# Kernel tuning notes

Hardware: AMD Instinct MI355X
Metric: run time of the kernel (lower is better)

## Reference

```python
import jax, jax.numpy as jnp
import numpy as np


def _ln(x, g, b):
    m = x.mean(-1, keepdims=True)
    v = ((x - m) ** 2).mean(-1, keepdims=True)
    return (x - m) * jax.lax.rsqrt(v + 1e-5) * g + b


def _forward(x, fx_in, pre_w1, pre_b1, pre_w2, pre_b2, placeholder,
             ln1_g, ln1_b, px_w, px_b, pfx_w, pfx_b, slice_w, slice_b, temp,
             q_w, k_w, v_w, out_w, out_b, ln2_g, ln2_b,
             mlp_w1, mlp_b1, mlp_w2, mlp_b2,
             ln3_g, ln3_b, head_w1, head_b1, head_w2, head_b2):
    # All linear weights are stored as [in, out] (pre-transposed vs torch nn.Linear).
    B, N, _ = x.shape
    L, H = temp.shape
    dh = slice_w.shape[1]
    gelu = lambda t: jax.nn.gelu(t, approximate=False)
    # preprocess MLP (n_layers=0, res=False): Linear -> GELU -> Linear
    h = jnp.concatenate([x, fx_in], axis=-1)
    h = gelu(h @ pre_w1 + pre_b1) @ pre_w2 + pre_b2
    h = h + placeholder  # learned [D] offset
    scale = 1.0 / jnp.sqrt(jnp.asarray(dh, h.dtype))
    for i in range(L):  # loop over structurally distinct layers
        y = _ln(h, ln1_g[i], ln1_b[i])
        # project to per-head features: bhnd
        fx_mid = (y @ pfx_w[i] + pfx_b[i]).reshape(B, N, H, dh).transpose(0, 2, 1, 3)
        x_mid = (y @ px_w[i] + px_b[i]).reshape(B, N, H, dh).transpose(0, 2, 1, 3)
        # soft slice assignment over G slices
        logits = jnp.einsum('bhnd,dg->bhng', x_mid, slice_w[i]) + slice_b[i]
        sw = jax.nn.softmax(logits / temp[i][None, :, None, None], axis=-1)  # bhng
        norm = sw.sum(axis=2)  # bhg
        tok = jnp.einsum('bhnd,bhng->bhgd', fx_mid, sw) / (norm + 1e-5)[..., None]
        # attention over G=slice_num tokens
        q = tok @ q_w[i]
        k = tok @ k_w[i]
        v = tok @ v_w[i]
        attn = jax.nn.softmax(jnp.einsum('bhgd,bhmd->bhgm', q, k) * scale, axis=-1)
        out_slice = jnp.einsum('bhgm,bhmd->bhgd', attn, v)
        # deslice back to points
        out_x = jnp.einsum('bhgd,bhng->bhnd', out_slice, sw)
        out_x = out_x.transpose(0, 2, 1, 3).reshape(B, N, H * dh)
        h = h + (out_x @ out_w[i] + out_b[i])
        z = _ln(h, ln2_g[i], ln2_b[i])
        h = h + (gelu(z @ mlp_w1[i] + mlp_b1[i]) @ mlp_w2[i] + mlp_b2[i])
    z = _ln(h, ln3_g, ln3_b)
    return gelu(z @ head_w1 + head_b1) @ head_w2 + head_b2


def setup_inputs() -> dict:
    key = jax.random.key(0)
    B, N, D, H, dh, G, L = 2, 16384, 256, 8, 32, 64, 5
    SP, FUN, OUT = 2, 4, 4
    ID = H * dh  # inner_dim == n_hidden
    MR = D * 1   # mlp_ratio=1
    ks = iter(jax.random.split(key, 64))
    nrm = lambda shape, s=0.02: jax.random.normal(next(ks), shape, jnp.float32) * s
    return dict(
        x=jax.random.normal(next(ks), (B, N, SP), jnp.float32),
        fx_in=jax.random.normal(next(ks), (B, N, FUN), jnp.float32),
        pre_w1=nrm((SP + FUN, 2 * D)), pre_b1=jnp.zeros((2 * D,), jnp.float32),
        pre_w2=nrm((2 * D, D)), pre_b2=jnp.zeros((D,), jnp.float32),
        placeholder=nrm((D,)),
        ln1_g=jnp.ones((L, D), jnp.float32), ln1_b=jnp.zeros((L, D), jnp.float32),
        px_w=nrm((L, D, ID)), px_b=jnp.zeros((L, ID), jnp.float32),
        pfx_w=nrm((L, D, ID)), pfx_b=jnp.zeros((L, ID), jnp.float32),
        slice_w=nrm((L, dh, G), 0.1), slice_b=jnp.zeros((L, G), jnp.float32),
        temp=0.5 * jnp.ones((L, H), jnp.float32),
        q_w=nrm((L, dh, dh), 0.1), k_w=nrm((L, dh, dh), 0.1), v_w=nrm((L, dh, dh), 0.1),
        out_w=nrm((L, ID, D)), out_b=jnp.zeros((L, D), jnp.float32),
        ln2_g=jnp.ones((L, D), jnp.float32), ln2_b=jnp.zeros((L, D), jnp.float32),
        mlp_w1=nrm((L, D, MR)), mlp_b1=jnp.zeros((L, MR), jnp.float32),
        mlp_w2=nrm((L, MR, D)), mlp_b2=jnp.zeros((L, D), jnp.float32),
        ln3_g=jnp.ones((D,), jnp.float32), ln3_b=jnp.zeros((D,), jnp.float32),
        head_w1=nrm((D, D)), head_b1=jnp.zeros((D,), jnp.float32),
        head_w2=nrm((D, OUT)), head_b2=jnp.zeros((OUT,), jnp.float32),
    )


def reference(x, fx_in, pre_w1, pre_b1, pre_w2, pre_b2, placeholder,
              ln1_g, ln1_b, px_w, px_b, pfx_w, pfx_b, slice_w, slice_b, temp,
              q_w, k_w, v_w, out_w, out_b, ln2_g, ln2_b,
              mlp_w1, mlp_b1, mlp_w2, mlp_b2,
              ln3_g, ln3_b, head_w1, head_b1, head_w2, head_b2):
    return _forward(x, fx_in, pre_w1, pre_b1, pre_w2, pre_b2, placeholder,
                    ln1_g, ln1_b, px_w, px_b, pfx_w, pfx_b, slice_w, slice_b, temp,
                    q_w, k_w, v_w, out_w, out_b, ln2_g, ln2_b,
                    mlp_w1, mlp_b1, mlp_w2, mlp_b2,
                    ln3_g, ln3_b, head_w1, head_b1, head_w2, head_b2)
```

## Files before the change

kernel.cpp:

```cpp
#include <hip/hip_runtime.h>


#define MTOK 32768
#define NB   16384

typedef unsigned short u16;
using short8 = __attribute__((ext_vector_type(8))) short;
using f4     = __attribute__((ext_vector_type(4))) float;

__device__ __forceinline__ float bfu(u16 u) {
    return __uint_as_float(((unsigned)u) << 16);
}
__device__ __forceinline__ u16 f2bf(float f) {
    unsigned u = __float_as_uint(f);
    u += 0x7FFFu + ((u >> 16) & 1u);
    return (u16)(u >> 16);
}
__device__ __forceinline__ float ldf(const void* p, int i, int isbf) {
    return isbf ? bfu(((const u16*)p)[i]) : ((const float*)p)[i];
}
__device__ __forceinline__ float4 dec4(ushort4 u) {
    return make_float4(bfu(u.x), bfu(u.y), bfu(u.z), bfu(u.w));
}
__device__ __forceinline__ float gelu_f(float x) {
    return 0.5f * x * (1.0f + erff(x * 0.7071067811865475f));
}

#define F_H      ((size_t)0)
#define F_TOK    ((size_t)8388608)
#define F_NORM   ((size_t)8421376)
#define F_OS     ((size_t)8422400)
#define F_BIAS   ((size_t)8455168)
#define F_PARAMS ((size_t)8463360)
#define F_BF     ((size_t)8696196)
#define B_PB2C 0
#define B_PFXB 256
#define B_OUTB 1536
#define B_M1B  2816
#define B_M2B  4096
#define B_HB1  5376
#define B_SL   5632
#define B_END  8192
#define U_WT     ((size_t)0)
#define WT_PRE2  0
#define WT_HEAD1 131072
#define WT_PXSL  196608
#define WT_PFX   851968
#define WT_OUT   1179648
#define WT_MLP1  1507328
#define WT_MLP2  1835008
#define WT_END   2162688
#define U_Y   ((size_t)2162688)
#define U_XM  ((size_t)10551296)
#define U_FM  ((size_t)18939904)
#define U_SW  ((size_t)27328512)

#define P_X    0
#define P_FX   65536
#define P_W1   196608
#define P_B1   199680
#define P_LN1G 200192
#define P_LN1B 201472
#define P_LN2G 202752
#define P_LN2B 204032
#define P_LN3G 205312
#define P_LN3B 205568
#define P_SLW  205824
#define P_SLB  216064
#define P_TEMP 216384
#define P_QW   216448
#define P_KW   221568
#define P_VW   226688
#define P_HW2  231808
#define P_HB2  232832
#define P_END  232836

__global__ __launch_bounds__(256) void cvt_kernel(
    const void* x, const void* fx, const void* w1, const void* b1,
    const void* l1g, const void* l1b, const void* l2g, const void* l2b,
    const void* l3g, const void* l3b, const void* slw, const void* slb,
    const void* tmp, const void* qw, const void* kw, const void* vw,
    const void* hw2, const void* hb2, float* __restrict__ P)
{
    int isbf = (((const u16*)tmp)[0] != 0);
    int idx = blockIdx.x * 256 + threadIdx.x;
    const void* s; int o;
    if      (idx < 65536)  { s = x;   o = idx; }
    else if (idx < 196608) { s = fx;  o = idx - 65536; }
    else if (idx < 199680) { s = w1;  o = idx - 196608; }
    else if (idx < 200192) { s = b1;  o = idx - 199680; }
    else if (idx < 201472) { s = l1g; o = idx - 200192; }
    else if (idx < 202752) { s = l1b; o = idx - 201472; }
    else if (idx < 204032) { s = l2g; o = idx - 202752; }
    else if (idx < 205312) { s = l2b; o = idx - 204032; }
    else if (idx < 205568) { s = l3g; o = idx - 205312; }
    else if (idx < 205824) { s = l3b; o = idx - 205568; }
    else if (idx < 216064) { s = slw; o = idx - 205824; }
    else if (idx < 216384) { s = slb; o = idx - 216064; }
    else if (idx < 216424) { s = tmp; o = idx - 216384; }
    else if (idx < 216448) { return; }
    else if (idx < 221568) { s = qw;  o = idx - 216448; }
    else if (idx < 226688) { s = kw;  o = idx - 221568; }
    else if (idx < 231808) { s = vw;  o = idx - 226688; }
    else if (idx < 232832) { s = hw2; o = idx - 231808; }
    else if (idx < 232836) { s = hb2; o = idx - 232832; }
    else return;
    P[idx] = ldf(s, o, isbf);
}

__global__ __launch_bounds__(256) void prep_kernel(
    const void* pre_w2, const void* head_w1, const void* px_w, const void* pfx_w,
    const void* out_w, const void* mlp_w1, const void* mlp_w2, const void* pre_b2,
    const void* placeholder, const void* px_b, const void* pfx_b, const void* out_b,
    const void* mlp_b1, const void* mlp_b2, const void* head_b1,
    const void* slw, const void* slb, const void* tmp,
    u16* __restrict__ WT, float* __restrict__ BIAS)
{
    int isbf = (((const u16*)tmp)[0] != 0);
    int idx = blockIdx.x * 256 + threadIdx.x;
    if (idx < 131072) {
        int n = idx >> 9, k = idx & 511;
        WT[idx] = f2bf(ldf(pre_w2, k * 256 + n, isbf));
    } else if (idx < WT_PXSL) {
        int f = idx - 131072;
        int n = f >> 8, k = f & 255;
        WT[idx] = f2bf(ldf(head_w1, k * 256 + n, isbf));
    } else if (idx < WT_PFX) {
        int f = idx - WT_PXSL;
        int i = f / 131072, r = f % 131072;
        int n = r >> 8, k = r & 255;
        int h = n >> 6, g = n & 63;
        float a = 0.f;
#pragma unroll
        for (int d = 0; d < 32; ++d)
            a = fmaf(ldf(px_w, i * 65536 + k * 256 + h * 32 + d, isbf),
                     ldf(slw, i * 2048 + d * 64 + g, isbf), a);
        WT[idx] = f2bf(a);
    } else if (idx < WT_END) {
        int f = idx - WT_PFX;
        int mat = f >> 16;
        int r = f & 65535;
        const void* s; int off = (mat % 5) * 65536;
        if      (mat < 5)  s = pfx_w;
        else if (mat < 10) s = out_w;
        else if (mat < 15) s = mlp_w1;
        else               s = mlp_w2;
        int n = r >> 8, k = r & 255;
        WT[idx] = f2bf(ldf(s, off + k * 256 + n, isbf));
    } else if (idx < WT_END + 256) {
        int c = idx - WT_END;
        BIAS[B_PB2C + c] = ldf(pre_b2, c, isbf) + ldf(placeholder, c, isbf);
    } else if (idx < WT_END + B_SL) {
        int o = idx - (WT_END + 256);
        float v;
        if      (o < 1280) v = ldf(pfx_b,  o,        isbf);
        else if (o < 2560) v = ldf(out_b,  o - 1280, isbf);
        else if (o < 3840) v = ldf(mlp_b1, o - 2560, isbf);
        else if (o < 5120) v = ldf(mlp_b2, o - 3840, isbf);
        else               v = ldf(head_b1, o - 5120, isbf);
        BIAS[B_PFXB + o] = v;
    } else if (idx < WT_END + B_END) {
        int o = idx - (WT_END + B_SL);
        int i = o >> 9, n = o & 511;
        int h = n >> 6, g = n & 63;
        float a = ldf(slb, i * 64 + g, isbf);
#pragma unroll
        for (int d = 0; d < 32; ++d)
            a = fmaf(ldf(px_b, i * 256 + h * 32 + d, isbf),
                     ldf(slw, i * 2048 + d * 64 + g, isbf), a);
        BIAS[B_SL + o] = a;
    }
}

__global__ __launch_bounds__(256) void pre1_kernel(
    const float* __restrict__ P, u16* __restrict__ HID)
{
    int idx = blockIdx.x * 256 + threadIdx.x;
    int m = idx >> 9, j = idx & 511;
    const float* xx = P + P_X;
    const float* ff = P + P_FX;
    const float* w1 = P + P_W1;
    float a = P[P_B1 + j];
    a = fmaf(xx[m * 2 + 0], w1[0 * 512 + j], a);
    a = fmaf(xx[m * 2 + 1], w1[1 * 512 + j], a);
    a = fmaf(ff[m * 4 + 0], w1[2 * 512 + j], a);
    a = fmaf(ff[m * 4 + 1], w1[3 * 512 + j], a);
    a = fmaf(ff[m * 4 + 2], w1[4 * 512 + j], a);
    a = fmaf(ff[m * 4 + 3], w1[5 * 512 + j], a);
    HID[idx] = f2bf(gelu_f(a));
}

template <int KK, int OMODE>
__global__ __launch_bounds__(256, 2) void gemm_mfma(
    const u16* __restrict__ A, const u16* __restrict__ Wt,
    const float* __restrict__ bias, float* __restrict__ C, u16* __restrict__ Cb)
{
    __shared__ u16 As[128 * 72];
    __shared__ u16 Bs[128 * 72];
    const int t = threadIdx.x;
    const int wave = t >> 6, lane = t & 63;
    const int quad = lane >> 4, l15 = lane & 15;
    const int m0 = blockIdx.x * 128;
    const int n0 = blockIdx.y * 128;
    const int wm = (wave & 1) * 64, wn = (wave >> 1) * 64;
    f4 acc[4][4];
#pragma unroll
    for (int i = 0; i < 4; ++i)
#pragma unroll
        for (int j = 0; j < 4; ++j)
            acc[i][j] = (f4){0.f, 0.f, 0.f, 0.f};

    for (int kc = 0; kc < KK; kc += 64) {
        if (kc) __syncthreads();
#pragma unroll
        for (int i = 0; i < 4; ++i) {
            int c = t + 256 * i;
            int row = c >> 3, col = (c & 7) * 8;
            *(ulonglong2*)(As + row * 72 + col) =
                *(const ulonglong2*)(A + (size_t)(m0 + row) * KK + kc + col);
            *(ulonglong2*)(Bs + row * 72 + col) =
                *(const ulonglong2*)(Wt + (size_t)(n0 + row) * KK + kc + col);
        }
        __syncthreads();
#pragma unroll
        for (int k32 = 0; k32 < 64; k32 += 32) {
            short8 a[4], b[4];
#pragma unroll
            for (int i = 0; i < 4; ++i)
                a[i] = *(const short8*)(As + (wm + i * 16 + l15) * 72 + k32 + quad * 8);
#pragma unroll
            for (int j = 0; j < 4; ++j)
                b[j] = *(const short8*)(Bs + (wn + j * 16 + l15) * 72 + k32 + quad * 8);
#pragma unroll
            for (int i = 0; i < 4; ++i)
#pragma unroll
                for (int j = 0; j < 4; ++j)
                    acc[i][j] = __builtin_amdgcn_mfma_f32_16x16x32_bf16(
                        a[i], b[j], acc[i][j], 0, 0, 0);
        }
    }
#pragma unroll
    for (int j = 0; j < 4; ++j) {
        int cj = n0 + wn + j * 16 + l15;
        float bj = bias[cj];
#pragma unroll
        for (int i = 0; i < 4; ++i) {
            int rbase = m0 + wm + i * 16 + quad * 4;
#pragma unroll
            for (int r = 0; r < 4; ++r) {
                float v = acc[i][j][r] + bj;
                size_t off = (size_t)(rbase + r) * 256 + cj;
                if (OMODE == 3) v = gelu_f(v);
                if (OMODE == 1) v += C[off];
                if (OMODE >= 2) Cb[off] = f2bf(v);
                else            C[off] = v;
            }
        }
    }
}

__global__ __launch_bounds__(256, 2) void gemm_slice(
    const u16* __restrict__ A, const u16* __restrict__ Wt,
    const float* __restrict__ bsl, const float* __restrict__ tempv,
    u16* __restrict__ SW)
{
    __shared__ u16 As[128 * 72];
    __shared__ u16 Bs[128 * 72];
    const int t = threadIdx.x;
    const int wave = t >> 6, lane = t & 63;
    const int quad = lane >> 4, l15 = lane & 15;
    const int m0 = blockIdx.x * 128;
    const int n0 = blockIdx.y * 128;
    const int wm = (wave & 1) * 64, wn = (wave >> 1) * 64;
    f4 acc[4][4];
#pragma unroll
    for (int i = 0; i < 4; ++i)
#pragma unroll
        for (int j = 0; j < 4; ++j)
            acc[i][j] = (f4){0.f, 0.f, 0.f, 0.f};

    for (int kc = 0; kc < 256; kc += 64) {
        if (kc) __syncthreads();
#pragma unroll
        for (int i = 0; i < 4; ++i) {
            int c = t + 256 * i;
            int row = c >> 3, col = (c & 7) * 8;
            *(ulonglong2*)(As + row * 72 + col) =
                *(const ulonglong2*)(A + (size_t)(m0 + row) * 256 + kc + col);
            *(ulonglong2*)(Bs + row * 72 + col) =
                *(const ulonglong2*)(Wt + (size_t)(n0 + row) * 256 + kc + col);
        }
        __syncthreads();
#pragma unroll
        for (int k32 = 0; k32 < 64; k32 += 32) {
            short8 a[4], b[4];
#pragma unroll
            for (int i = 0; i < 4; ++i)
                a[i] = *(const short8*)(As + (wm + i * 16 + l15) * 72 + k32 + quad * 8);
#pragma unroll
            for (int j = 0; j < 4; ++j)
                b[j] = *(const short8*)(Bs + (wn + j * 16 + l15) * 72 + k32 + quad * 8);
#pragma unroll
            for (int i = 0; i < 4; ++i)
#pragma unroll
                for (int j = 0; j < 4; ++j)
                    acc[i][j] = __builtin_amdgcn_mfma_f32_16x16x32_bf16(
                        a[i], b[j], acc[i][j], 0, 0, 0);
        }
    }
    const int h = (n0 + wn) >> 6;
    const float itemp = 1.0f / tempv[h];
    float bj[4];
#pragma unroll
    for (int j = 0; j < 4; ++j) bj[j] = bsl[n0 + wn + j * 16 + l15];
#pragma unroll
    for (int i = 0; i < 4; ++i) {
#pragma unroll
        for (int r = 0; r < 4; ++r) {
            float v[4];
            float mx = -3.0e38f;
#pragma unroll
            for (int j = 0; j < 4; ++j) {
                v[j] = (acc[i][j][r] + bj[j]) * itemp;
                mx = fmaxf(mx, v[j]);
            }
#pragma unroll
            for (int o = 1; o < 16; o <<= 1) mx = fmaxf(mx, __shfl_xor(mx, o));
            float s = 0.f;
#pragma unroll
            for (int j = 0; j < 4; ++j) { v[j] = expf(v[j] - mx); s += v[j]; }
#pragma unroll
            for (int o = 1; o < 16; o <<= 1) s += __shfl_xor(s, o);
            float inv = 1.0f / s;
            int m = m0 + wm + i * 16 + quad * 4 + r;
            int b = m >> 14, n = m & 16383;
            size_t base = (((size_t)(b * 8 + h)) * NB + n) * 64;
#pragma unroll
            for (int j = 0; j < 4; ++j)
                SW[base + j * 16 + l15] = f2bf(v[j] * inv);
        }
    }
}

__global__ __launch_bounds__(256) void ln_kernel(
    const float* __restrict__ X, const float* __restrict__ g,
    const float* __restrict__ b, u16* __restrict__ Y)
{
    int lane = threadIdx.x & 63;
    size_t m = (size_t)blockIdx.x * 4 + (threadIdx.x >> 6);
    const float4 x4 = *(const float4*)(X + m * 256 + lane * 4);
    float s = x4.x + x4.y + x4.z + x4.w;
    float q = x4.x * x4.x + x4.y * x4.y + x4.z * x4.z + x4.w * x4.w;
#pragma unroll
    for (int o = 32; o; o >>= 1) { s += __shfl_xor(s, o); q += __shfl_xor(q, o); }
    float mean = s * (1.0f / 256.0f);
    float var = q * (1.0f / 256.0f) - mean * mean;
    float inv = 1.0f / sqrtf(var + 1e-5f);
    const float4 g4 = *(const float4*)(g + lane * 4);
    const float4 b4 = *(const float4*)(b + lane * 4);
    ushort4 y;
    y.x = f2bf((x4.x - mean) * inv * g4.x + b4.x);
    y.y = f2bf((x4.y - mean) * inv * g4.y + b4.y);
    y.z = f2bf((x4.z - mean) * inv * g4.z + b4.z);
    y.w = f2bf((x4.w - mean) * inv * g4.w + b4.w);
    *(ushort4*)(Y + m * 256 + lane * 4) = y;
}

__global__ __launch_bounds__(256) void tok_kernel(
    const u16* __restrict__ FM, const u16* __restrict__ SW,
    float* __restrict__ TOK, float* __restrict__ NORM)
{
    int bh = blockIdx.x >> 6, chunk = blockIdx.x & 63;
    int b = bh >> 3, hd = bh & 7;
    int t = threadIdx.x, wave = t >> 6, lane = t & 63;
    int g0 = (lane >> 3) * 8, d0 = (lane & 7) * 4;
    float4 acc[8];
#pragma unroll
    for (int gi = 0; gi < 8; ++gi) acc[gi] = make_float4(0.f, 0.f, 0.f, 0.f);
    float4 n0a = make_float4(0.f, 0.f, 0.f, 0.f);
    float4 n1a = make_float4(0.f, 0.f, 0.f, 0.f);
    int nbase = chunk * 256 + wave * 64;
    const u16* fmB = FM + ((size_t)b * NB + nbase) * 256 + hd * 32 + d0;
    const u16* swB = SW + ((size_t)bh * NB + nbase) * 64 + g0;
    for (int j = 0; j < 64; ++j) {
        float4 f4v = dec4(*(const ushort4*)(fmB + (size_t)j * 256));
        float4 s0 = dec4(*(const ushort4*)(swB + (size_t)j * 64));
        float4 s1 = dec4(*(const ushort4*)(swB + (size_t)j * 64 + 4));
#define TOKACC(gi, sv)                                            \
        acc[gi].x = fmaf(f4v.x, sv, acc[gi].x);                   \
        acc[gi].y = fmaf(f4v.y, sv, acc[gi].y);                   \
        acc[gi].z = fmaf(f4v.z, sv, acc[gi].z);                   \
        acc[gi].w = fmaf(f4v.w, sv, acc[gi].w);
        TOKACC(0, s0.x) TOKACC(1, s0.y) TOKACC(2, s0.z) TOKACC(3, s0.w)
        TOKACC(4, s1.x) TOKACC(5, s1.y) TOKACC(6, s1.z) TOKACC(7, s1.w)
#undef TOKACC
        n0a.x += s0.x; n0a.y += s0.y; n0a.z += s0.z; n0a.w += s0.w;
        n1a.x += s1.x; n1a.y += s1.y; n1a.z += s1.z; n1a.w += s1.w;
    }
    __shared__ float red[4][2048];
    __shared__ float nred[4][64];
#pragma unroll
    for (int gi = 0; gi < 8; ++gi)
        *(float4*)&red[wave][(g0 + gi) * 32 + d0] = acc[gi];
    if ((lane & 7) == 0) {
        nred[wave][g0 + 0] = n0a.x; nred[wave][g0 + 1] = n0a.y;
        nred[wave][g0 + 2] = n0a.z; nred[wave][g0 + 3] = n0a.w;
        nred[wave][g0 + 4] = n1a.x; nred[wave][g0 + 5] = n1a.y;
        nred[wave][g0 + 6] = n1a.z; nred[wave][g0 + 7] = n1a.w;
    }
    __syncthreads();
    size_t tokBase = (size_t)bh * 2048;
#pragma unroll
    for (int k = 0; k < 8; ++k) {
        int c = t + 256 * k;
        atomicAdd(&TOK[tokBase + c], red[0][c] + red[1][c] + red[2][c] + red[3][c]);
    }
    if (t < 64)
        atomicAdd(&NORM[bh * 64 + t], nred[0][t] + nred[1][t] + nred[2][t] + nred[3][t]);
}

__global__ __launch_bounds__(256) void attn_kernel(
    const float* __restrict__ TOK, const float* __restrict__ NORM,
    const float* __restrict__ qw, const float* __restrict__ kw,
    const float* __restrict__ vw, float* __restrict__ OS)
{
    __shared__ float tokd[2048], qs[2048], ks[2048], vs[2048];
    int bh = blockIdx.x;
    int t = threadIdx.x;
#pragma unroll
    for (int i = 0; i < 2; ++i) {
        int f4v = t + 256 * i;
        float4 v = *(const float4*)(TOK + (size_t)bh * 2048 + f4v * 4);
        float inv = 1.0f / (NORM[bh * 64 + (f4v >> 3)] + 1e-5f);
        v.x *= inv; v.y *= inv; v.z *= inv; v.w *= inv;
        *(float4*)&tokd[f4v * 4] = v;
    }
    __syncthreads();
#pragma unroll
    for (int i = 0; i < 8; ++i) {
        int f = t + 256 * i;
        int g = f >> 5, d = f & 31;
        const float* tr = tokd + g * 32;
        float aq = 0.f, ak = 0.f, av = 0.f;
#pragma unroll
        for (int e = 0; e < 32; ++e) {
            float tv = tr[e];
            aq = fmaf(tv, qw[e * 32 + d], aq);
            ak = fmaf(tv, kw[e * 32 + d], ak);
            av = fmaf(tv, vw[e * 32 + d], av);
        }
        qs[f] = aq; ks[f] = ak; vs[f] = av;
    }
    __syncthreads();
    int g = t >> 2, sub = t & 3;
    float4 qv[8];
#pragma unroll
    for (int e4 = 0; e4 < 8; ++e4) qv[e4] = *(const float4*)(qs + g * 32 + e4 * 4);
    float p[16];
    float mx = -3.0e38f;
#pragma unroll
    for (int mm = 0; mm < 16; ++mm) {
        int mI = sub * 16 + mm;
        const float4* kr = (const float4*)(ks + mI * 32);
        float s = 0.f;
#pragma unroll
        for (int e4 = 0; e4 < 8; ++e4) {
            float4 kv = kr[e4];
            s = fmaf(qv[e4].x, kv.x, s); s = fmaf(qv[e4].y, kv.y, s);
// ... 105 lines not shown
        if (isbf) {
            ushort4 r; r.x = f2bf(o0); r.y = f2bf(o1); r.z = f2bf(o2); r.w = f2bf(o3);
            *(ushort4*)((u16*)OUT + m * 4) = r;
        } else {
            *(float4*)((float*)OUT + m * 4) = make_float4(o0, o1, o2, o3);
        }
    }
}

extern "C" void kernel_launch(void* const* d_in, const int* in_sizes, int n_in,
                              void* d_out, int out_size, void* d_ws, size_t ws_size,
                              hipStream_t stream)
{
    const void* x = d_in[0];      const void* fx = d_in[1];
    const void* pre_w1 = d_in[2]; const void* pre_b1 = d_in[3];
    const void* pre_w2 = d_in[4]; const void* pre_b2 = d_in[5];
    const void* placeholder = d_in[6];
    const void* ln1_g = d_in[7];  const void* ln1_b = d_in[8];
    const void* px_w = d_in[9];   const void* px_b = d_in[10];
    const void* pfx_w = d_in[11]; const void* pfx_b = d_in[12];
    const void* slice_w = d_in[13]; const void* slice_b = d_in[14];
    const void* temp = d_in[15];
    const void* q_w = d_in[16];   const void* k_w = d_in[17]; const void* v_w = d_in[18];
    const void* out_w = d_in[19]; const void* out_b = d_in[20];
    const void* ln2_g = d_in[21]; const void* ln2_b = d_in[22];
    const void* mlp_w1 = d_in[23]; const void* mlp_b1 = d_in[24];
    const void* mlp_w2 = d_in[25]; const void* mlp_b2 = d_in[26];
    const void* ln3_g = d_in[27]; const void* ln3_b = d_in[28];
    const void* head_w1 = d_in[29]; const void* head_b1 = d_in[30];
    const void* head_w2 = d_in[31]; const void* head_b2 = d_in[32];

    float* ws = (float*)d_ws;
    float* H     = ws + F_H;
    float* TOKp  = ws + F_TOK;
    float* NORMp = ws + F_NORM;
    float* OSp   = ws + F_OS;
    float* BIAS  = ws + F_BIAS;
    float* P     = ws + F_PARAMS;
    u16*   U     = (u16*)(ws + F_BF);
    u16*   WT    = U + U_WT;
    u16*   Yb    = U + U_Y;
    u16*   XMb   = U + U_XM;
    u16*   FMb   = U + U_FM;
    u16*   SWb   = U + U_SW;
    u16*   HIDb  = U + U_XM;

    cvt_kernel<<<910, 256, 0, stream>>>(x, fx, pre_w1, pre_b1, ln1_g, ln1_b,
        ln2_g, ln2_b, ln3_g, ln3_b, slice_w, slice_b, temp, q_w, k_w, v_w,
        head_w2, head_b2, P);
    prep_kernel<<<8480, 256, 0, stream>>>(pre_w2, head_w1, px_w, pfx_w, out_w,
        mlp_w1, mlp_w2, pre_b2, placeholder, px_b, pfx_b, out_b, mlp_b1, mlp_b2,
        head_b1, slice_w, slice_b, temp, WT, BIAS);
    pre1_kernel<<<65536, 256, 0, stream>>>(P, HIDb);

    dim3 gg(256, 2);
    dim3 gs(256, 4);
    gemm_mfma<512, 0><<<gg, 256, 0, stream>>>(HIDb, WT + WT_PRE2, BIAS + B_PB2C, H, nullptr);

    for (int i = 0; i < 5; ++i) {
        ln_kernel<<<8192, 256, 0, stream>>>(H, P + P_LN1G + i * 256, P + P_LN1B + i * 256, Yb);
        gemm_slice<<<gs, 256, 0, stream>>>(Yb, WT + WT_PXSL + i * 131072, BIAS + B_SL + i * 512, P + P_TEMP + i * 8, SWb);
        gemm_mfma<256, 2><<<gg, 256, 0, stream>>>(Yb, WT + WT_PFX + i * 65536, BIAS + B_PFXB + i * 256, nullptr, FMb);
        hipMemsetAsync(TOKp, 0, (size_t)33792 * 4, stream);
        tok_kernel<<<1024, 256, 0, stream>>>(FMb, SWb, TOKp, NORMp);
        attn_kernel<<<16, 256, 0, stream>>>(TOKp, NORMp, P + P_QW + i * 1024, P + P_KW + i * 1024, P + P_VW + i * 1024, OSp);
        deslice_kernel<<<2048, 256, 0, stream>>>(OSp, SWb, Yb);
        gemm_mfma<256, 1><<<gg, 256, 0, stream>>>(Yb, WT + WT_OUT + i * 65536, BIAS + B_OUTB + i * 256, H, nullptr);
        ln_kernel<<<8192, 256, 0, stream>>>(H, P + P_LN2G + i * 256, P + P_LN2B + i * 256, Yb);
        gemm_mfma<256, 3><<<gg, 256, 0, stream>>>(Yb,  WT + WT_MLP1 + i * 65536, BIAS + B_M1B + i * 256, nullptr, XMb);
        gemm_mfma<256, 1><<<gg, 256, 0, stream>>>(XMb, WT + WT_MLP2 + i * 65536, BIAS + B_M2B + i * 256, H, nullptr);
    }

    ln_kernel<<<8192, 256, 0, stream>>>(H, P + P_LN3G, P + P_LN3B, Yb);
    gemm_mfma<256, 3><<<gg, 256, 0, stream>>>(Yb, WT + WT_HEAD1, BIAS + B_HB1, nullptr, XMb);
    head2_kernel<<<8192, 256, 0, stream>>>(XMb, P + P_HW2, P + P_HB2, temp, d_out);
}
```

Baseline: 1.265 ms.

## Fuse layernorm into GEMM epilogues, merge slice/fx projections, drop token atomics

Residual GEMMs now compute full 256-wide rows per block, so the following LayerNorm runs in the epilogue and the standalone ln_kernel launches go away. The slice-logit and fx projections are merged into one GEMM with a concatenated weight. Token reduction writes per-chunk partials that attn_kernel sums, replacing the memset and atomics. Also adds an XOR-swizzled LDS layout, vectorized pre1, and a tiled weight-prep kernel. The risks are lower occupancy from the wider GEMM tiles and the extra partial-sum reads in attn.

New measurement: 1.851 ms. 1.46x slower.

```diff
diff --git a/kernel.cpp b/kernel.cpp
--- a/kernel.cpp
+++ b/kernel.cpp
@@ -27,25 +27,23 @@
 }
 
 #define F_H      ((size_t)0)
-#define F_TOK    ((size_t)8388608)
-#define F_NORM   ((size_t)8421376)
-#define F_OS     ((size_t)8422400)
-#define F_BIAS   ((size_t)8455168)
-#define F_PARAMS ((size_t)8463360)
-#define F_BF     ((size_t)8696196)
+#define F_OS     ((size_t)8388608)
+#define F_TOKP   ((size_t)8421376)
+#define F_NORMP  ((size_t)8945664)
+#define F_BIAS   ((size_t)8962048)
+#define F_PARAMS ((size_t)8970240)
+#define F_BF     ((size_t)9203076)
 #define B_PB2C 0
-#define B_PFXB 256
-#define B_OUTB 1536
-#define B_M1B  2816
-#define B_M2B  4096
-#define B_HB1  5376
-#define B_SL   5632
+#define B_OUTB 256
+#define B_M1B  1536
+#define B_M2B  2816
+#define B_HB1  4096
+#define B_SP   4352
 #define B_END  8192
 #define U_WT     ((size_t)0)
 #define WT_PRE2  0
 #define WT_HEAD1 131072
-#define WT_PXSL  196608
-#define WT_PFX   851968
+#define WT_SPFX  196608
 #define WT_OUT   1179648
 #define WT_MLP1  1507328
 #define WT_MLP2  1835008
@@ -108,95 +106,238 @@
     P[idx] = ldf(s, o, isbf);
 }
 
-__global__ __launch_bounds__(256) void prep_kernel(
-    const void* pre_w2, const void* head_w1, const void* px_w, const void* pfx_w,
-    const void* out_w, const void* mlp_w1, const void* mlp_w2, const void* pre_b2,
-    const void* placeholder, const void* px_b, const void* pfx_b, const void* out_b,
-    const void* mlp_b1, const void* mlp_b2, const void* head_b1,
-    const void* slw, const void* slb, const void* tmp,
+__global__ __launch_bounds__(256) void prep_main(
+    const void* pre_w2, const void* head_w1, const void* pfx_w,
+    const void* out_w, const void* mlp_w1, const void* mlp_w2,
+    const void* pre_b2, const void* placeholder, const void* pfx_b,
+    const void* out_b, const void* mlp_b1, const void* mlp_b2,
+    const void* head_b1, const void* tmp,
     u16* __restrict__ WT, float* __restrict__ BIAS)
 {
     int isbf = (((const u16*)tmp)[0] != 0);
     int idx = blockIdx.x * 256 + threadIdx.x;
     if (idx < 131072) {
         int n = idx >> 9, k = idx & 511;
-        WT[idx] = f2bf(ldf(pre_w2, k * 256 + n, isbf));
-    } else if (idx < WT_PXSL) {
+        WT[WT_PRE2 + idx] = f2bf(ldf(pre_w2, k * 256 + n, isbf));
+    } else if (idx < 196608) {
         int f = idx - 131072;
         int n = f >> 8, k = f & 255;
-        WT[idx] = f2bf(ldf(head_w1, k * 256 + n, isbf));
-    } else if (idx < WT_PFX) {
-        int f = idx - WT_PXSL;
-        int i = f / 131072, r = f % 131072;
+        WT[WT_HEAD1 + f] = f2bf(ldf(head_w1, k * 256 + n, isbf));
+    } else if (idx < 524288) {
+        int f = idx - 196608;
+        int i = f >> 16, r = f & 65535;
         int n = r >> 8, k = r & 255;
-        int h = n >> 6, g = n & 63;
-        float a = 0.f;
-#pragma unroll
-        for (int d = 0; d < 32; ++d)
-            a = fmaf(ldf(px_w, i * 65536 + k * 256 + h * 32 + d, isbf),
-                     ldf(slw, i * 2048 + d * 64 + g, isbf), a);
-        WT[idx] = f2bf(a);
-    } else if (idx < WT_END) {
-        int f = idx - WT_PFX;
-        int mat = f >> 16;
-        int r = f & 65535;
+        WT[WT_SPFX + (size_t)i * 196608 + (512 + n) * 256 + k] =
+            f2bf(ldf(pfx_w, i * 65536 + k * 256 + n, isbf));
+    } else if (idx < 1507328) {
+        int f = idx - 524288;
+        int mat = f >> 16, r = f & 65535;
         const void* s; int off = (mat % 5) * 65536;
-        if      (mat < 5)  s = pfx_w;
-        else if (mat < 10) s = out_w;
-        else if (mat < 15) s = mlp_w1;
+        if      (mat < 5)  s = out_w;
+        else if (mat < 10) s = mlp_w1;
         else               s = mlp_w2;
         int n = r >> 8, k = r & 255;
-        WT[idx] = f2bf(ldf(s, off + k * 256 + n, isbf));
-    } else if (idx < WT_END + 256) {
-        int c = idx - WT_END;
+        WT[WT_OUT + f] = f2bf(ldf(s, off + k * 256 + n, isbf));
+    } else if (idx < 1507584) {
+        int c = idx - 1507328;
         BIAS[B_PB2C + c] = ldf(pre_b2, c, isbf) + ldf(placeholder, c, isbf);
-    } else if (idx < WT_END + B_SL) {
-        int o = idx - (WT_END + 256);
-        float v;
-        if      (o < 1280) v = ldf(pfx_b,  o,        isbf);
-        else if (o < 2560) v = ldf(out_b,  o - 1280, isbf);
-        else if (o < 3840) v = ldf(mlp_b1, o - 2560, isbf);
-        else if (o < 5120) v = ldf(mlp_b2, o - 3840, isbf);
-        else               v = ldf(head_b1, o - 5120, isbf);
-        BIAS[B_PFXB + o] = v;
-    } else if (idx < WT_END + B_END) {
-        int o = idx - (WT_END + B_SL);
-        int i = o >> 9, n = o & 511;
-        int h = n >> 6, g = n & 63;
+    } else if (idx < 1508864) {
+        int o = idx - 1507584; BIAS[B_OUTB + o] = ldf(out_b, o, isbf);
+    } else if (idx < 1510144) {
+        int o = idx - 1508864; BIAS[B_M1B + o] = ldf(mlp_b1, o, isbf);
+    } else if (idx < 1511424) {
+        int o = idx - 1510144; BIAS[B_M2B + o] = ldf(mlp_b2, o, isbf);
+    } else if (idx < 1511680) {
+        int o = idx - 1511424; BIAS[B_HB1 + o] = ldf(head_b1, o, isbf);
+    } else if (idx < 1512960) {
+        int o = idx - 1511680;
+        int i = o >> 8, c = o & 255;
+        BIAS[B_SP + i * 768 + 512 + c] = ldf(pfx_b, o, isbf);
+    }
+}
+
+__global__ __launch_bounds__(256) void prep_pxsl(
+    const void* px_w, const void* px_b, const void* slw, const void* slb,
+    const void* tmp, u16* __restrict__ WT, float* __restrict__ BIAS)
+{
+    int isbf = (((const u16*)tmp)[0] != 0);
+    __shared__ float pxs[64 * 33];
+    __shared__ float sls[2048];
+    int blk = blockIdx.x;
+    int i = blk >> 5, h = (blk >> 2) & 7, kb = blk & 3;
+    int t = threadIdx.x;
+#pragma unroll
+    for (int p = 0; p < 8; ++p) {
+        int flat = t + 256 * p;
+        sls[flat] = ldf(slw, i * 2048 + flat, isbf);
+        int k = flat >> 5, d = flat & 31;
+        pxs[k * 33 + d] = ldf(px_w, i * 65536 + (kb * 64 + k) * 256 + h * 32 + d, isbf);
+    }
+    __syncthreads();
+    int k = t & 63, gb = t >> 6;
+    float acc[16];
+#pragma unroll
+    for (int gi = 0; gi < 16; ++gi) acc[gi] = 0.f;
+#pragma unroll
+    for (int d = 0; d < 32; ++d) {
+        float pv = pxs[k * 33 + d];
+        const float* sp = sls + d * 64 + gb * 16;
+#pragma unroll
+        for (int gi = 0; gi < 16; ++gi) acc[gi] = fmaf(pv, sp[gi], acc[gi]);
+    }
+    u16* WTp = WT + WT_SPFX + (size_t)i * 196608;
+#pragma unroll
+    for (int gi = 0; gi < 16; ++gi) {
+        int n = h * 64 + gb * 16 + gi;
+        WTp[n * 256 + kb * 64 + k] = f2bf(acc[gi]);
+    }
+    if (kb == 0 && t < 64) {
+        int g = t;
         float a = ldf(slb, i * 64 + g, isbf);
 #pragma unroll
         for (int d = 0; d < 32; ++d)
-            a = fmaf(ldf(px_b, i * 256 + h * 32 + d, isbf),
-                     ldf(slw, i * 2048 + d * 64 + g, isbf), a);
-        BIAS[B_SL + o] = a;
+            a = fmaf(ldf(px_b, i * 256 + h * 32 + d, isbf), sls[d * 64 + g], a);
+        BIAS[B_SP + i * 768 + h * 64 + g] = a;
     }
 }
 
 __global__ __launch_bounds__(256) void pre1_kernel(
     const float* __restrict__ P, u16* __restrict__ HID)
 {
-    int idx = blockIdx.x * 256 + threadIdx.x;
-    int m = idx >> 9, j = idx & 511;
-    const float* xx = P + P_X;
-    const float* ff = P + P_FX;
+    int base = (blockIdx.x * 256 + threadIdx.x) * 8;
+    int m = base >> 9, j0 = base & 511;
     const float* w1 = P + P_W1;
-    float a = P[P_B1 + j];
-    a = fmaf(xx[m * 2 + 0], w1[0 * 512 + j], a);
-    a = fmaf(xx[m * 2 + 1], w1[1 * 512 + j], a);
-    a = fmaf(ff[m * 4 + 0], w1[2 * 512 + j], a);
-    a = fmaf(ff[m * 4 + 1], w1[3 * 512 + j], a);
-    a = fmaf(ff[m * 4 + 2], w1[4 * 512 + j], a);
-    a = fmaf(ff[m * 4 + 3], w1[5 * 512 + j], a);
-    HID[idx] = f2bf(gelu_f(a));
-}
-
-template <int KK, int OMODE>
-__global__ __launch_bounds__(256, 2) void gemm_mfma(
+    float xa = P[P_X + m * 2], xb = P[P_X + m * 2 + 1];
+    float fa = P[P_FX + m * 4], fb = P[P_FX + m * 4 + 1];
+    float fc = P[P_FX + m * 4 + 2], fd = P[P_FX + m * 4 + 3];
+    u16 outv[8];
+#pragma unroll
+    for (int jj = 0; jj < 8; ++jj) {
+        int j = j0 + jj;
+        float a = P[P_B1 + j];
+        a = fmaf(xa, w1[j], a);
+        a = fmaf(xb, w1[512 + j], a);
+        a = fmaf(fa, w1[1024 + j], a);
+        a = fmaf(fb, w1[1536 + j], a);
+        a = fmaf(fc, w1[2048 + j], a);
+        a = fmaf(fd, w1[2560 + j], a);
+        outv[jj] = f2bf(gelu_f(a));
+    }
+    *(ushort4*)(HID + base)     = make_ushort4(outv[0], outv[1], outv[2], outv[3]);
+    *(ushort4*)(HID + base + 4) = make_ushort4(outv[4], outv[5], outv[6], outv[7]);
+}
+
+template <int KK, bool RES>
+__global__ __launch_bounds__(256, 3) void gemm_ln(
     const u16* __restrict__ A, const u16* __restrict__ Wt,
-    const float* __restrict__ bias, float* __restrict__ C, u16* __restrict__ Cb)
-{
-    __shared__ u16 As[128 * 72];
-    __shared__ u16 Bs[128 * 72];
+    const float* __restrict__ bias, const float* __restrict__ lng,
+    const float* __restrict__ lnb, float* __restrict__ H, u16* __restrict__ Y)
+{
+    __shared__ u16 As[64 * 64];
+    __shared__ u16 Bs[256 * 64];
+    __shared__ float rs[2][64], rq[2][64];
+    const int t = threadIdx.x;
+    const int wave = t >> 6, lane = t & 63;
+    const int quad = lane >> 4, l15 = lane & 15;
+    const int m0 = blockIdx.x * 64;
+    const int wm = (wave & 1) * 32, wn = (wave >> 1) * 128;
+    f4 acc[2][8];
+#pragma unroll
+    for (int i = 0; i < 2; ++i)
+#pragma unroll
+        for (int j = 0; j < 8; ++j) acc[i][j] = (f4){0.f, 0.f, 0.f, 0.f};
+
+    for (int kc = 0; kc < KK; kc += 64) {
+        if (kc) __syncthreads();
+#pragma unroll
+        for (int p = 0; p < 2; ++p) {
+            int c = t + 256 * p;
+            int row = c >> 3, c8 = c & 7;
+            *(ulonglong2*)(As + row * 64 + ((c8 ^ (row & 7)) << 3)) =
+                *(const ulonglong2*)(A + (size_t)(m0 + row) * KK + kc + c8 * 8);
+        }
+#pragma unroll
+        for (int p = 0; p < 8; ++p) {
+            int c = t + 256 * p;
+            int row = c >> 3, c8 = c & 7;
+            *(ulonglong2*)(Bs + row * 64 + ((c8 ^ (row & 7)) << 3)) =
+                *(const ulonglong2*)(Wt + (size_t)row * KK + kc + c8 * 8);
+        }
+        __syncthreads();
+#pragma unroll
+        for (int kk = 0; kk < 2; ++kk) {
+            short8 a[2], b[8];
+#pragma unroll
+            for (int i = 0; i < 2; ++i) {
+                int R = wm + i * 16 + l15;
+                a[i] = *(const short8*)(As + R * 64 + (((quad + kk * 4) ^ (R & 7)) << 3));
+            }
+#pragma unroll
+            for (int j = 0; j < 8; ++j) {
+                int R = wn + j * 16 + l15;
+                b[j] = *(const short8*)(Bs + R * 64 + (((quad + kk * 4) ^ (R & 7)) << 3));
+            }
+#pragma unroll
+            for (int i = 0; i < 2; ++i)
+#pragma unroll
+                for (int j = 0; j < 8; ++j)
+                    acc[i][j] = __builtin_amdgcn_mfma_f32_16x16x32_bf16(
+                        a[i], b[j], acc[i][j], 0, 0, 0);
+        }
+    }
+    float bj[8];
+    int colj[8];
+#pragma unroll
+    for (int j = 0; j < 8; ++j) { colj[j] = wn + j * 16 + l15; bj[j] = bias[colj[j]]; }
+    const int half = wn >> 7;
+#pragma unroll
+    for (int i = 0; i < 2; ++i) {
+#pragma unroll
+        for (int r = 0; r < 4; ++r) {
+            int row = wm + i * 16 + quad * 4 + r;
+            size_t gbase = (size_t)(m0 + row) * 256;
+            float s = 0.f, q = 0.f;
+#pragma unroll
+            for (int j = 0; j < 8; ++j) {
+                float v = acc[i][j][r] + bj[j];
+                if (RES) v += H[gbase + colj[j]];
+                H[gbase + colj[j]] = v;
+                acc[i][j][r] = v;
+                s += v; q += v * v;
+            }
+#pragma unroll
+            for (int o = 1; o < 16; o <<= 1) { s += __shfl_xor(s, o); q += __shfl_xor(q, o); }
+            if (l15 == 0) { rs[half][row] = s; rq[half][row] = q; }
+        }
+    }
+    __syncthreads();
+    float gj[8], betj[8];
+#pragma unroll
+    for (int j = 0; j < 8; ++j) { gj[j] = lng[colj[j]]; betj[j] = lnb[colj[j]]; }
+#pragma unroll
+    for (int i = 0; i < 2; ++i) {
+#pragma unroll
+        for (int r = 0; r < 4; ++r) {
+            int row = wm + i * 16 + quad * 4 + r;
+            size_t gbase = (size_t)(m0 + row) * 256;
+            float mean = (rs[0][row] + rs[1][row]) * (1.0f / 256.0f);
+            float var = (rq[0][row] + rq[1][row]) * (1.0f / 256.0f) - mean * mean;
+            float rstd = rsqrtf(var + 1e-5f);
+#pragma unroll
+            for (int j = 0; j < 8; ++j) {
+                float y = (acc[i][j][r] - mean) * rstd * gj[j] + betj[j];
+                Y[gbase + colj[j]] = f2bf(y);
+            }
+        }
+    }
+}
+
+__global__ __launch_bounds__(256, 4) void gemm_gelu(
+    const u16* __restrict__ A, const u16* __restrict__ Wt,
+    const float* __restrict__ bias, u16* __restrict__ Cb)
+{
+    __shared__ u16 As[128 * 64];
+    __shared__ u16 Bs[128 * 64];
     const int t = threadIdx.x;
     const int wave = t >> 6, lane = t & 63;
     const int quad = lane >> 4, l15 = lane & 15;
@@ -207,30 +348,34 @@
 #pragma unroll
     for (int i = 0; i < 4; ++i)
 #pragma unroll
-        for (int j = 0; j < 4; ++j)
-            acc[i][j] = (f4){0.f, 0.f, 0.f, 0.f};
-
-    for (int kc = 0; kc < KK; kc += 64) {
+        for (int j = 0; j < 4; ++j) acc[i][j] = (f4){0.f, 0.f, 0.f, 0.f};
+
+    for (int kc = 0; kc < 256; kc += 64) {
         if (kc) __syncthreads();
 #pragma unroll
-        for (int i = 0; i < 4; ++i) {
-            int c = t + 256 * i;
-            int row = c >> 3, col = (c & 7) * 8;
-            *(ulonglong2*)(As + row * 72 + col) =
-                *(const ulonglong2*)(A + (size_t)(m0 + row) * KK + kc + col);
-            *(ulonglong2*)(Bs + row * 72 + col) =
-                *(const ulonglong2*)(Wt + (size_t)(n0 + row) * KK + kc + col);
+        for (int p = 0; p < 4; ++p) {
+            int c = t + 256 * p;
+            int row = c >> 3, c8 = c & 7;
+            int off = row * 64 + ((c8 ^ (row & 7)) << 3);
+            *(ulonglong2*)(As + off) =
+                *(const ulonglong2*)(A + (size_t)(m0 + row) * 256 + kc + c8 * 8);
+            *(ulonglong2*)(Bs + off) =
+                *(const ulonglong2*)(Wt + (size_t)(n0 + row) * 256 + kc + c8 * 8);
         }
         __syncthreads();
 #pragma unroll
-        for (int k32 = 0; k32 < 64; k32 += 32) {
+        for (int kk = 0; kk < 2; ++kk) {
             short8 a[4], b[4];
 #pragma unroll
-            for (int i = 0; i < 4; ++i)
-                a[i] = *(const short8*)(As + (wm + i * 16 + l15) * 72 + k32 + quad * 8);
-#pragma unroll
-            for (int j = 0; j < 4; ++j)
-                b[j] = *(const short8*)(Bs + (wn + j * 16 + l15) * 72 + k32 + quad * 8);
+            for (int i = 0; i < 4; ++i) {
+                int R = wm + i * 16 + l15;
+                a[i] = *(const short8*)(As + R * 64 + (((quad + kk * 4) ^ (R & 7)) << 3));
+            }
+#pragma unroll
+            for (int j = 0; j < 4; ++j) {
+                int R = wn + j * 16 + l15;
+                b[j] = *(const short8*)(Bs + R * 64 + (((quad + kk * 4) ^ (R & 7)) << 3));
+            }
 #pragma unroll
             for (int i = 0; i < 4; ++i)
 #pragma unroll
@@ -248,24 +393,20 @@
             int rbase = m0 + wm + i * 16 + quad * 4;
 #pragma unroll
             for (int r = 0; r < 4; ++r) {
-                float v = acc[i][j][r] + bj;
-                size_t off = (size_t)(rbase + r) * 256 + cj;
-                if (OMODE == 3) v = gelu_f(v);
-                if (OMODE == 1) v += C[off];
-                if (OMODE >= 2) Cb[off] = f2bf(v);
-                else            C[off] = v;
-            }
-        }
-    }
-}
-
-__global__ __launch_bounds__(256, 2) void gemm_slice(
+                float v = gelu_f(acc[i][j][r] + bj);
+                Cb[(size_t)(rbase + r) * 256 + cj] = f2bf(v);
+            }
+        }
+    }
+}
+
+__global__ __launch_bounds__(256, 4) void gemm_spfx(
     const u16* __restrict__ A, const u16* __restrict__ Wt,
-    const float* __restrict__ bsl, const float* __restrict__ tempv,
-    u16* __restrict__ SW)
-{
-    __shared__ u16 As[128 * 72];
-    __shared__ u16 Bs[128 * 72];
+    const float* __restrict__ bsp, const float* __restrict__ tempv,
+    u16* __restrict__ SW, u16* __restrict__ FM)
+{
+    __shared__ u16 As[128 * 64];
+    __shared__ u16 Bs[128 * 64];
     const int t = threadIdx.x;
     const int wave = t >> 6, lane = t & 63;
     const int quad = lane >> 4, l15 = lane & 15;
@@ -276,30 +417,34 @@
 #pragma unroll
     for (int i = 0; i < 4; ++i)
 #pragma unroll
-        for (int j = 0; j < 4; ++j)
-            acc[i][j] = (f4){0.f, 0.f, 0.f, 0.f};
+        for (int j = 0; j < 4; ++j) acc[i][j] = (f4){0.f, 0.f, 0.f, 0.f};
 
     for (int kc = 0; kc < 256; kc += 64) {
         if (kc) __syncthreads();
 #pragma unroll
-        for (int i = 0; i < 4; ++i) {
-            int c = t + 256 * i;
-            int row = c >> 3, col = (c & 7) * 8;
-            *(ulonglong2*)(As + row * 72 + col) =
-                *(const ulonglong2*)(A + (size_t)(m0 + row) * 256 + kc + col);
-            *(ulonglong2*)(Bs + row * 72 + col) =
-                *(const ulonglong2*)(Wt + (size_t)(n0 + row) * 256 + kc + col);
+        for (int p = 0; p < 4; ++p) {
+            int c = t + 256 * p;
+            int row = c >> 3, c8 = c & 7;
+            int off = row * 64 + ((c8 ^ (row & 7)) << 3);
+            *(ulonglong2*)(As + off) =
+                *(const ulonglong2*)(A + (size_t)(m0 + row) * 256 + kc + c8 * 8);
+            *(ulonglong2*)(Bs + off) =
+                *(const ulonglong2*)(Wt + (size_t)(n0 + row) * 256 + kc + c8 * 8);
         }
         __syncthreads();
 #pragma unroll
-        for (int k32 = 0; k32 < 64; k32 += 32) {
+        for (int kk = 0; kk < 2; ++kk) {
             short8 a[4], b[4];
 #pragma unroll
-            for (int i = 0; i < 4; ++i)
-                a[i] = *(const short8*)(As + (wm + i * 16 + l15) * 72 + k32 + quad * 8);
-#pragma unroll
-            for (int j = 0; j < 4; ++j)
-                b[j] = *(const short8*)(Bs + (wn + j * 16 + l15) * 72 + k32 + quad * 8);
+            for (int i = 0; i < 4; ++i) {
+                int R = wm + i * 16 + l15;
+                a[i] = *(const short8*)(As + R * 64 + (((quad + kk * 4) ^ (R & 7)) << 3));
+            }
+#pragma unroll
+            for (int j = 0; j < 4; ++j) {
+                int R = wn + j * 16 + l15;
+                b[j] = *(const short8*)(Bs + R * 64 + (((quad + kk * 4) ^ (R & 7)) << 3));
+            }
 #pragma unroll
             for (int i = 0; i < 4; ++i)
 #pragma unroll
@@ -308,69 +453,60 @@
                         a[i], b[j], acc[i][j], 0, 0, 0);
         }
     }
-    const int h = (n0 + wn) >> 6;
-    const float itemp = 1.0f / tempv[h];
     float bj[4];
 #pragma unroll
-    for (int j = 0; j < 4; ++j) bj[j] = bsl[n0 + wn + j * 16 + l15];
-#pragma unroll
-    for (int i = 0; i < 4; ++i) {
-#pragma unroll
-        for (int r = 0; r < 4; ++r) {
-            float v[4];
-            float mx = -3.0e38f;
-#pragma unroll
-            for (int j = 0; j < 4; ++j) {
-                v[j] = (acc[i][j][r] + bj[j]) * itemp;
-                mx = fmaxf(mx, v[j]);
-            }
-#pragma unroll
-            for (int o = 1; o < 16; o <<= 1) mx = fmaxf(mx, __shfl_xor(mx, o));
-            float s = 0.f;
-#pragma unroll
-            for (int j = 0; j < 4; ++j) { v[j] = expf(v[j] - mx); s += v[j]; }
-#pragma unroll
-            for (int o = 1; o < 16; o <<= 1) s += __shfl_xor(s, o);
-            float inv = 1.0f / s;
-            int m = m0 + wm + i * 16 + quad * 4 + r;
-            int b = m >> 14, n = m & 16383;
-            size_t base = (((size_t)(b * 8 + h)) * NB + n) * 64;
-#pragma unroll
-            for (int j = 0; j < 4; ++j)
-                SW[base + j * 16 + l15] = f2bf(v[j] * inv);
-        }
-    }
-}
-
-__global__ __launch_bounds__(256) void ln_kernel(
-    const float* __restrict__ X, const float* __restrict__ g,
-    const float* __restrict__ b, u16* __restrict__ Y)
-{
-    int lane = threadIdx.x & 63;
-    size_t m = (size_t)blockIdx.x * 4 + (threadIdx.x >> 6);
-    const float4 x4 = *(const float4*)(X + m * 256 + lane * 4);
-    float s = x4.x + x4.y + x4.z + x4.w;
-    float q = x4.x * x4.x + x4.y * x4.y + x4.z * x4.z + x4.w * x4.w;
-#pragma unroll
-    for (int o = 32; o; o >>= 1) { s += __shfl_xor(s, o); q += __shfl_xor(q, o); }
-    float mean = s * (1.0f / 256.0f);
-    float var = q * (1.0f / 256.0f) - mean * mean;
-    float inv = 1.0f / sqrtf(var + 1e-5f);
-    const float4 g4 = *(const float4*)(g + lane * 4);
-    const float4 b4 = *(const float4*)(b + lane * 4);
-    ushort4 y;
-    y.x = f2bf((x4.x - mean) * inv * g4.x + b4.x);
-    y.y = f2bf((x4.y - mean) * inv * g4.y + b4.y);
-    y.z = f2bf((x4.z - mean) * inv * g4.z + b4.z);
-    y.w = f2bf((x4.w - mean) * inv * g4.w + b4.w);
-    *(ushort4*)(Y + m * 256 + lane * 4) = y;
-}
-
-__global__ __launch_bounds__(256) void tok_kernel(
+    for (int j = 0; j < 4; ++j) bj[j] = bsp[n0 + wn + j * 16 + l15];
+    if (blockIdx.y < 4) {
+        const int h = (n0 + wn) >> 6;
+        const float itemp = 1.0f / tempv[h];
+#pragma unroll
+        for (int i = 0; i < 4; ++i) {
+#pragma unroll
+            for (int r = 0; r < 4; ++r) {
+                float v[4];
+                float mx = -3.0e38f;
+#pragma unroll
+                for (int j = 0; j < 4; ++j) {
+                    v[j] = (acc[i][j][r] + bj[j]) * itemp;
+                    mx = fmaxf(mx, v[j]);
+                }
+#pragma unroll
+                for (int o = 1; o < 16; o <<= 1) mx = fmaxf(mx, __shfl_xor(mx, o));
+                float s = 0.f;
+#pragma unroll
+                for (int j = 0; j < 4; ++j) { v[j] = expf(v[j] - mx); s += v[j]; }
+#pragma unroll
+                for (int o = 1; o < 16; o <<= 1) s += __shfl_xor(s, o);
+                float inv = 1.0f / s;
+                int m = m0 + wm + i * 16 + quad * 4 + r;
+                int b = m >> 14, n = m & 16383;
+                size_t base = (((size_t)(b * 8 + h)) * NB + n) * 64;
+#pragma unroll
+                for (int j = 0; j < 4; ++j)
+                    SW[base + j * 16 + l15] = f2bf(v[j] * inv);
+            }
+        }
+    } else {
+        int cj = (n0 - 512) + wn + l15;
+#pragma unroll
+        for (int j = 0; j < 4; ++j) {
+            int col = cj + j * 16;
+#pragma unroll
+            for (int i = 0; i < 4; ++i) {
+                int rbase = m0 + wm + i * 16 + quad * 4;
+#pragma unroll
+                for (int r = 0; r < 4; ++r)
+                    FM[(size_t)(rbase + r) * 256 + col] = f2bf(acc[i][j][r] + bj[j]);
+            }
+        }
+    }
+}
+
+__global__ __launch_bounds__(256) void tok1_kernel(
     const u16* __restrict__ FM, const u16* __restrict__ SW,
-    float* __restrict__ TOK, float* __restrict__ NORM)
-{
-    int bh = blockIdx.x >> 6, chunk = blockIdx.x & 63;
+    float* __restrict__ TOKP, float* __restrict__ NORMP)
+{
+    int bh = blockIdx.x >> 4, chunk = blockIdx.x & 15;
     int b = bh >> 3, hd = bh & 7;
     int t = threadIdx.x, wave = t >> 6, lane = t & 63;
     int g0 = (lane >> 3) * 8, d0 = (lane & 7) * 4;
@@ -379,23 +515,25 @@
     for (int gi = 0; gi < 8; ++gi) acc[gi] = make_float4(0.f, 0.f, 0.f, 0.f);
     float4 n0a = make_float4(0.f, 0.f, 0.f, 0.f);
     float4 n1a = make_float4(0.f, 0.f, 0.f, 0.f);
-    int nbase = chunk * 256 + wave * 64;
-    const u16* fmB = FM + ((size_t)b * NB + nbase) * 256 + hd * 32 + d0;
-    const u16* swB = SW + ((size_t)bh * NB + nbase) * 64 + g0;
-    for (int j = 0; j < 64; ++j) {
-        float4 f4v = dec4(*(const ushort4*)(fmB + (size_t)j * 256));
-        float4 s0 = dec4(*(const ushort4*)(swB + (size_t)j * 64));
-        float4 s1 = dec4(*(const ushort4*)(swB + (size_t)j * 64 + 4));
+    for (int pass = 0; pass < 4; ++pass) {
+        int nbase = chunk * 1024 + pass * 256 + wave * 64;
+        const u16* fmB = FM + ((size_t)b * NB + nbase) * 256 + hd * 32 + d0;
+        const u16* swB = SW + ((size_t)bh * NB + nbase) * 64 + g0;
+        for (int j = 0; j < 64; ++j) {
+            float4 f4v = dec4(*(const ushort4*)(fmB + (size_t)j * 256));
+            float4 s0 = dec4(*(const ushort4*)(swB + (size_t)j * 64));
+            float4 s1 = dec4(*(const ushort4*)(swB + (size_t)j * 64 + 4));
 #define TOKACC(gi, sv)                                            \
-        acc[gi].x = fmaf(f4v.x, sv, acc[gi].x);                   \
-        acc[gi].y = fmaf(f4v.y, sv, acc[gi].y);                   \
-        acc[gi].z = fmaf(f4v.z, sv, acc[gi].z);                   \
-        acc[gi].w = fmaf(f4v.w, sv, acc[gi].w);
-        TOKACC(0, s0.x) TOKACC(1, s0.y) TOKACC(2, s0.z) TOKACC(3, s0.w)
-        TOKACC(4, s1.x) TOKACC(5, s1.y) TOKACC(6, s1.z) TOKACC(7, s1.w)
+            acc[gi].x = fmaf(f4v.x, sv, acc[gi].x);               \
+            acc[gi].y = fmaf(f4v.y, sv, acc[gi].y);               \
+            acc[gi].z = fmaf(f4v.z, sv, acc[gi].z);               \
+            acc[gi].w = fmaf(f4v.w, sv, acc[gi].w);
+            TOKACC(0, s0.x) TOKACC(1, s0.y) TOKACC(2, s0.z) TOKACC(3, s0.w)
+            TOKACC(4, s1.x) TOKACC(5, s1.y) TOKACC(6, s1.z) TOKACC(7, s1.w)
 #undef TOKACC
-        n0a.x += s0.x; n0a.y += s0.y; n0a.z += s0.z; n0a.w += s0.w;
-        n1a.x += s1.x; n1a.y += s1.y; n1a.z += s1.z; n1a.w += s1.w;
+            n0a.x += s0.x; n0a.y += s0.y; n0a.z += s0.z; n0a.w += s0.w;
+            n1a.x += s1.x; n1a.y += s1.y; n1a.z += s1.z; n1a.w += s1.w;
+        }
     }
     __shared__ float red[4][2048];
     __shared__ float nred[4][64];
@@ -409,31 +547,39 @@
         nred[wave][g0 + 6] = n1a.z; nred[wave][g0 + 7] = n1a.w;
     }
     __syncthreads();
-    size_t tokBase = (size_t)bh * 2048;
+    size_t tokBase = (size_t)(chunk * 16 + bh) * 2048;
 #pragma unroll
     for (int k = 0; k < 8; ++k) {
         int c = t + 256 * k;
-        atomicAdd(&TOK[tokBase + c], red[0][c] + red[1][c] + red[2][c] + red[3][c]);
+        TOKP[tokBase + c] = red[0][c] + red[1][c] + red[2][c] + red[3][c];
     }
     if (t < 64)
-        atomicAdd(&NORM[bh * 64 + t], nred[0][t] + nred[1][t] + nred[2][t] + nred[3][t]);
+        NORMP[(chunk * 16 + bh) * 64 + t] = nred[0][t] + nred[1][t] + nred[2][t] + nred[3][t];
 }
 
 __global__ __launch_bounds__(256) void attn_kernel(
-    const float* __restrict__ TOK, const float* __restrict__ NORM,
+    const float* __restrict__ TOKP, const float* __restrict__ NORMP,
     const float* __restrict__ qw, const float* __restrict__ kw,
     const float* __restrict__ vw, float* __restrict__ OS)
 {
     __shared__ float tokd[2048], qs[2048], ks[2048], vs[2048];
+    __shared__ float nrm[64];
     int bh = blockIdx.x;
     int t = threadIdx.x;
-#pragma unroll
-    for (int i = 0; i < 2; ++i) {
-        int f4v = t + 256 * i;
-        float4 v = *(const float4*)(TOK + (size_t)bh * 2048 + f4v * 4);
-        float inv = 1.0f / (NORM[bh * 64 + (f4v >> 3)] + 1e-5f);
-        v.x *= inv; v.y *= inv; v.z *= inv; v.w *= inv;
-        *(float4*)&tokd[f4v * 4] = v;
+    if (t < 64) {
+        float ns = 0.f;
+#pragma unroll
+        for (int ch = 0; ch < 16; ++ch) ns += NORMP[(ch * 16 + bh) * 64 + t];
+        nrm[t] = 1.0f / (ns + 1e-5f);
+    }
+    __syncthreads();
+#pragma unroll
+    for (int p = 0; p < 8; ++p) {
+        int c = t + 256 * p;
+        float s = 0.f;
+#pragma unroll
+        for (int ch = 0; ch < 16; ++ch) s += TOKP[(size_t)(ch * 16 + bh) * 2048 + c];
+        tokd[c] = s * nrm[c >> 5];
     }
     __syncthreads();
 #pragma unroll
@@ -605,9 +751,9 @@
 
     float* ws = (float*)d_ws;
     float* H     = ws + F_H;
-    float* TOKp  = ws + F_TOK;
-    float* NORMp = ws + F_NORM;
     float* OSp   = ws + F_OS;
+    float* TOKP  = ws + F_TOKP;
+    float* NORMP = ws + F_NORMP;
     float* BIAS  = ws + F_BIAS;
     float* P     = ws + F_PARAMS;
     u16*   U     = (u16*)(ws + F_BF);
@@ -621,30 +767,34 @@
     cvt_kernel<<<910, 256, 0, stream>>>(x, fx, pre_w1, pre_b1, ln1_g, ln1_b,
         ln2_g, ln2_b, ln3_g, ln3_b, slice_w, slice_b, temp, q_w, k_w, v_w,
         head_w2, head_b2, P);
-    prep_kernel<<<8480, 256, 0, stream>>>(pre_w2, head_w1, px_w, pfx_w, out_w,
-        mlp_w1, mlp_w2, pre_b2, placeholder, px_b, pfx_b, out_b, mlp_b1, mlp_b2,
-        head_b1, slice_w, slice_b, temp, WT, BIAS);
-    pre1_kernel<<<65536, 256, 0, stream>>>(P, HIDb);
-
-    dim3 gg(256, 2);
-    dim3 gs(256, 4);
-    gemm_mfma<512, 0><<<gg, 256, 0, stream>>>(HIDb, WT + WT_PRE2, BIAS + B_PB2C, H, nullptr);
-
+    prep_main<<<5910, 256, 0, stream>>>(pre_w2, head_w1, pfx_w, out_w, mlp_w1,
+        mlp_w2, pre_b2, placeholder, pfx_b, out_b, mlp_b1, mlp_b2, head_b1,
+        temp, WT, BIAS);
+    prep_pxsl<<<160, 256, 0, stream>>>(px_w, px_b, slice_w, slice_b, temp, WT, BIAS);
+    pre1_kernel<<<8192, 256, 0, stream>>>(P, HIDb);
+
+    gemm_ln<512, false><<<512, 256, 0, stream>>>(HIDb, WT + WT_PRE2,
+        BIAS + B_PB2C, P + P_LN1G, P + P_LN1B, H, Yb);
+
+    dim3 gsp(256, 6);
+    dim3 gpl(256, 2);
     for (int i = 0; i < 5; ++i) {
-        ln_kernel<<<8192, 256, 0, stream>>>(H, P + P_LN1G + i * 256, P + P_LN1B + i * 256, Yb);
-        gemm_slice<<<gs, 256, 0, stream>>>(Yb, WT + WT_PXSL + i * 131072, BIAS + B_SL + i * 512, P + P_TEMP + i * 8, SWb);
-        gemm_mfma<256, 2><<<gg, 256, 0, stream>>>(Yb, WT + WT_PFX + i * 65536, BIAS + B_PFXB + i * 256, nullptr, FMb);
-        hipMemsetAsync(TOKp, 0, (size_t)33792 * 4, stream);
-        tok_kernel<<<1024, 256, 0, stream>>>(FMb, SWb, TOKp, NORMp);
-        attn_kernel<<<16, 256, 0, stream>>>(TOKp, NORMp, P + P_QW + i * 1024, P + P_KW + i * 1024, P + P_VW + i * 1024, OSp);
+        gemm_spfx<<<gsp, 256, 0, stream>>>(Yb, WT + WT_SPFX + (size_t)i * 196608,
+            BIAS + B_SP + i * 768, P + P_TEMP + i * 8, SWb, FMb);
+        tok1_kernel<<<256, 256, 0, stream>>>(FMb, SWb, TOKP, NORMP);
+        attn_kernel<<<16, 256, 0, stream>>>(TOKP, NORMP, P + P_QW + i * 1024,
+            P + P_KW + i * 1024, P + P_VW + i * 1024, OSp);
         deslice_kernel<<<2048, 256, 0, stream>>>(OSp, SWb, Yb);
-        gemm_mfma<256, 1><<<gg, 256, 0, stream>>>(Yb, WT + WT_OUT + i * 65536, BIAS + B_OUTB + i * 256, H, nullptr);
-        ln_kernel<<<8192, 256, 0, stream>>>(H, P + P_LN2G + i * 256, P + P_LN2B + i * 256, Yb);
-        gemm_mfma<256, 3><<<gg, 256, 0, stream>>>(Yb,  WT + WT_MLP1 + i * 65536, BIAS + B_M1B + i * 256, nullptr, XMb);
-        gemm_mfma<256, 1><<<gg, 256, 0, stream>>>(XMb, WT + WT_MLP2 + i * 65536, BIAS + B_M2B + i * 256, H, nullptr);
-    }
-
-    ln_kernel<<<8192, 256, 0, stream>>>(H, P + P_LN3G, P + P_LN3B, Yb);
-    gemm_mfma<256, 3><<<gg, 256, 0, stream>>>(Yb, WT + WT_HEAD1, BIAS + B_HB1, nullptr, XMb);
+        gemm_ln<256, true><<<512, 256, 0, stream>>>(Yb, WT + WT_OUT + i * 65536,
+            BIAS + B_OUTB + i * 256, P + P_LN2G + i * 256, P + P_LN2B + i * 256, H, Yb);
+        gemm_gelu<<<gpl, 256, 0, stream>>>(Yb, WT + WT_MLP1 + i * 65536,
+            BIAS + B_M1B + i * 256, XMb);
+        const float* ng = (i < 4) ? (P + P_LN1G + (i + 1) * 256) : (P + P_LN3G);
+        const float* nb = (i < 4) ? (P + P_LN1B + (i + 1) * 256) : (P + P_LN3B);
+        gemm_ln<256, true><<<512, 256, 0, stream>>>(XMb, WT + WT_MLP2 + i * 65536,
+            BIAS + B_M2B + i * 256, ng, nb, H, Yb);
+    }
+
+    gemm_gelu<<<gpl, 256, 0, stream>>>(Yb, WT + WT_HEAD1, BIAS + B_HB1, XMb);
     head2_kernel<<<8192, 256, 0, stream>>>(XMb, P + P_HW2, P + P_HB2, temp, d_out);
 }
```
